# Kernel optimization log

Hardware: AMD Instinct MI355X
Metric: run time of the kernel (lower is better)

## Reference

```python
import jax, jax.numpy as jnp
import numpy as np

NEG = -1e30  # log-space 'zero' (avoid real -inf for stable exp/grad)


def _ctc_loss_mean(logp, targets, target_lengths, blank):
    """CTC loss, PyTorch semantics (reduction='mean', zero_infinity=True).
    logp: (B, T, V) log-probabilities; targets: (B, L) padded labels;
    target_lengths: (B,) ints. All input lengths are T (uniform here).
    """
    B, T, V = logp.shape
    L = targets.shape[1]
    S = 2 * L + 1  # extended label length: blank-interleaved

    ext = jnp.full((B, S), blank, dtype=targets.dtype)
    ext = ext.at[:, 1::2].set(targets)  # blanks at even s, labels at odd s

    s = jnp.arange(S)
    valid = s[None, :] < (2 * target_lengths + 1)[:, None]  # (B, S)
    prev2 = jnp.pad(ext[:, :-2], ((0, 0), (2, 0)), constant_values=blank)
    # skip transition s-2 -> s allowed only at non-blank s with no label repeat
    allow_skip = (s[None, :] >= 2) & (ext != blank) & (ext != prev2)

    # per-(t, s) emission log-prob, masked outside valid extended labels
    emit = jnp.take_along_axis(
        logp, jnp.broadcast_to(ext[:, None, :], (B, T, S)), axis=2
    )  # (B, T, S)
    emit = jnp.where(valid[:, None, :], emit, NEG)

    alpha0 = jnp.full((B, S), NEG, dtype=logp.dtype)
    alpha0 = alpha0.at[:, 0].set(emit[:, 0, 0])
    alpha0 = alpha0.at[:, 1].set(emit[:, 0, 1])

    def step(alpha, e):
        a1 = alpha
        a2 = jnp.pad(alpha[:, :-1], ((0, 0), (1, 0)), constant_values=NEG)
        a3 = jnp.pad(alpha[:, :-2], ((0, 0), (2, 0)), constant_values=NEG)
        a3 = jnp.where(allow_skip, a3, NEG)
        m = jnp.maximum(jnp.maximum(a1, a2), a3)
        new = m + jnp.log(jnp.exp(a1 - m) + jnp.exp(a2 - m) + jnp.exp(a3 - m)) + e
        return new, None

    alpha, _ = jax.lax.scan(step, alpha0, jnp.swapaxes(emit, 0, 1)[1:])

    i1 = (2 * target_lengths).astype(jnp.int32)
    l1 = jnp.take_along_axis(alpha, i1[:, None], axis=1)[:, 0]
    l2 = jnp.take_along_axis(alpha, jnp.maximum(i1 - 1, 0)[:, None], axis=1)[:, 0]
    l2 = jnp.where(target_lengths > 0, l2, NEG)
    m = jnp.maximum(l1, l2)
    loss = -(m + jnp.log(jnp.exp(l1 - m) + jnp.exp(l2 - m)))  # (B,)
    loss = jnp.where(loss > 1e20, 0.0, loss)  # zero_infinity=True
    # reduction='mean': divide by target length, then batch mean
    return jnp.mean(loss / jnp.maximum(target_lengths, 1).astype(loss.dtype))


def setup_inputs() -> dict:
    key = jax.random.key(0)
    kl, kt, kn = jax.random.split(key, 3)
    B, T, V, L = 32, 1024, 1000, 256
    logits = jax.random.normal(kl, (B, T, V), dtype=jnp.float32)
    targets = jax.random.randint(kt, (B, L), 1, V).astype(jnp.int32)
    lengths = jax.random.randint(kn, (B,), L // 2 + 2, L + 1)
    target_padding_mask = jnp.arange(L)[None, :] < lengths[:, None]  # bool (B, L)
    return {"logits": logits, "targets": targets,
            "target_padding_mask": target_padding_mask}


def reference(logits, targets, target_padding_mask):
    blank = 0
    lg = logits[:, :-1, :]            # drop last frame
    tgt = targets[:, 1:]              # drop leading (SOS) token
    logp = jax.nn.log_softmax(lg, axis=-1)  # (B, T-1, V)
    tlen = target_padding_mask.sum(axis=1).astype(jnp.int32) - 1
    return _ctc_loss_mean(logp, tgt, tlen, blank)
```

## Files before the change

### kernel.cpp

```cpp
#include <hip/hip_runtime.h>

#define LOG2E 1.4426950408889634f
#define LN2   0.6931471805599453

static constexpr int B  = 32;
static constexpr int T  = 1024;
static constexpr int TT = 1023;
static constexpr int V  = 1000;
static constexpr int L  = 256;
static constexpr int S  = 511;
static constexpr int SP = 512;
static constexpr int TP = 1024;

using h8  = __attribute__((ext_vector_type(8))) _Float16;
using hf2 = __attribute__((ext_vector_type(2))) __fp16;
using f4  = __attribute__((ext_vector_type(4))) float;
using i4  = __attribute__((ext_vector_type(4))) int;

__device__ __forceinline__ float fexp2(float x) {
#if __has_builtin(__builtin_amdgcn_exp2f)
  return __builtin_amdgcn_exp2f(x);
#else
  return exp2f(x);
#endif
}
__device__ __forceinline__ float flog2(float x) {
#if __has_builtin(__builtin_amdgcn_logf)
  return __builtin_amdgcn_logf(x);
#else
  return log2f(x);
#endif
}

#if __has_builtin(__builtin_amdgcn_update_dpp)
__device__ __forceinline__ float shr1f(float x) {
  int r = __builtin_amdgcn_update_dpp(0, __float_as_int(x), 0x138, 0xf, 0xf, true);
  return __int_as_float(r);
}
__device__ __forceinline__ int shl1i(int x) {
  return __builtin_amdgcn_update_dpp(0, x, 0x130, 0xf, 0xf, true);
}
#define DPP_SWITCH(T, OLD, SRC, BC)                                            \
  T r;                                                                         \
  switch (ctrl) {                                                              \
    case 0x111: r = __builtin_amdgcn_update_dpp(OLD, SRC, 0x111, 0xf, 0xf, BC); break; \
    case 0x112: r = __builtin_amdgcn_update_dpp(OLD, SRC, 0x112, 0xf, 0xf, BC); break; \
    case 0x114: r = __builtin_amdgcn_update_dpp(OLD, SRC, 0x114, 0xf, 0xf, BC); break; \
    case 0x118: r = __builtin_amdgcn_update_dpp(OLD, SRC, 0x118, 0xf, 0xf, BC); break; \
    case 0x142: r = __builtin_amdgcn_update_dpp(OLD, SRC, 0x142, 0xf, 0xf, BC); break; \
    default:    r = __builtin_amdgcn_update_dpp(OLD, SRC, 0x143, 0xf, 0xf, BC); break; \
  }

__device__ __forceinline__ int dppmax_step(int m, const int ctrl) {
  DPP_SWITCH(int, 0, m, true);
  return max(m, r);
}
__device__ __forceinline__ int wavemax_to_sgpr(int m) {
  m = dppmax_step(m, 0x111);
  m = dppmax_step(m, 0x112);
  m = dppmax_step(m, 0x114);
  m = dppmax_step(m, 0x118);
  m = dppmax_step(m, 0x142);
  m = dppmax_step(m, 0x143);
  return __builtin_amdgcn_readlane(m, 63);
}
__device__ __forceinline__ float dppfmax_step(float x, const int ctrl) {
  int xi = __float_as_int(x);
  DPP_SWITCH(int, xi, xi, false);
  return fmaxf(x, __int_as_float(r));
}
__device__ __forceinline__ float wavefmax(float x) {
  x = dppfmax_step(x, 0x111);
  x = dppfmax_step(x, 0x112);
  x = dppfmax_step(x, 0x114);
  x = dppfmax_step(x, 0x118);
  x = dppfmax_step(x, 0x142);
  x = dppfmax_step(x, 0x143);
  return __int_as_float(__builtin_amdgcn_readlane(__float_as_int(x), 63));
}
__device__ __forceinline__ float dppfadd_step(float x, const int ctrl) {
  DPP_SWITCH(int, 0, __float_as_int(x), true);
  return x + __int_as_float(r);
}
__device__ __forceinline__ float wavefsum(float x) {
  x = dppfadd_step(x, 0x111);
  x = dppfadd_step(x, 0x112);
  x = dppfadd_step(x, 0x114);
  x = dppfadd_step(x, 0x118);
  x = dppfadd_step(x, 0x142);
  x = dppfadd_step(x, 0x143);
  return __int_as_float(__builtin_amdgcn_readlane(__float_as_int(x), 63));
}
#else
__device__ __forceinline__ float shr1f(float x) {
  float r = __shfl_up(x, 1, 64);
  return (threadIdx.x & 63) == 0 ? 0.0f : r;
}
__device__ __forceinline__ int shl1i(int x) {
  int r = __shfl_down(x, 1, 64);
  return (threadIdx.x & 63) == 63 ? 0 : r;
}
__device__ __forceinline__ int wavemax_to_sgpr(int m) {
  for (int o = 32; o >= 1; o >>= 1) m = max(m, __shfl_xor(m, o, 64));
  return m;
}
__device__ __forceinline__ float wavefmax(float x) {
  for (int o = 32; o >= 1; o >>= 1) x = fmaxf(x, __shfl_xor(x, o, 64));
  return x;
}
__device__ __forceinline__ float wavefsum(float x) {
  for (int o = 32; o >= 1; o >>= 1) x += __shfl_xor(x, o, 64);
  return x;
}
#endif

__device__ __forceinline__ int mask_tlen(const unsigned char* maskb, int b, int lane) {
  int ca = 0;
  for (int k = lane; k < L; k += 64) ca += (maskb[b * L + k] != 0) ? 1 : 0;
  for (int o = 32; o >= 1; o >>= 1) ca += __shfl_xor(ca, o, 64);
  int cnt = ca;
  if (ca < 130) {
    const int* mi = (const int*)maskb;
    int cb = 0;
    for (int k = lane; k < L; k += 64) cb += (mi[b * L + k] != 0) ? 1 : 0;
    for (int o = 32; o >= 1; o >>= 1) cb += __shfl_xor(cb, o, 64);
    cnt = cb;
  }
  return cnt - 1;
}

__global__ __launch_bounds__(256) void k_emit(const float* __restrict__ logits,
                                              const int* __restrict__ targets,
                                              _Float16* __restrict__ E,
                                              float* __restrict__ G) {
  __shared__ float yrow[4][1024];
  const int wid = threadIdx.x >> 6;
  const int lane = threadIdx.x & 63;
  float* yw = yrow[wid];
  const int r = blockIdx.x * 4 + wid;
  const int b = r / TT;
  const int t = r - b * TT;

  const f4* row = reinterpret_cast<const f4*>(logits + ((size_t)b * T + t) * V);
  f4 u0 = row[lane];
  f4 u1 = row[lane + 64];
  f4 u2 = row[lane + 128];
  const bool has3 = (lane < 58);
  f4 u3;
  if (has3) u3 = row[lane + 192];
  else { u3[0] = u3[1] = u3[2] = u3[3] = -3.0e38f; }

  reinterpret_cast<f4*>(yw)[lane]       = u0;
  reinterpret_cast<f4*>(yw)[lane + 64]  = u1;
  reinterpret_cast<f4*>(yw)[lane + 128] = u2;
  if (has3) reinterpret_cast<f4*>(yw)[lane + 192] = u3;

  float lm = fmaxf(fmaxf(fmaxf(u0[0], u0[1]), fmaxf(u0[2], u0[3])),
                   fmaxf(fmaxf(u1[0], u1[1]), fmaxf(u1[2], u1[3])));
  lm = fmaxf(lm, fmaxf(fmaxf(u2[0], u2[1]), fmaxf(u2[2], u2[3])));
  lm = fmaxf(lm, fmaxf(fmaxf(u3[0], u3[1]), fmaxf(u3[2], u3[3])));
  const float my = wavefmax(lm);
  const float c = -my * LOG2E;

  float ps = fexp2(fmaf(u0[0], LOG2E, c)) + fexp2(fmaf(u0[1], LOG2E, c))
           + fexp2(fmaf(u0[2], LOG2E, c)) + fexp2(fmaf(u0[3], LOG2E, c))
           + fexp2(fmaf(u1[0], LOG2E, c)) + fexp2(fmaf(u1[1], LOG2E, c))
           + fexp2(fmaf(u1[2], LOG2E, c)) + fexp2(fmaf(u1[3], LOG2E, c))
           + fexp2(fmaf(u2[0], LOG2E, c)) + fexp2(fmaf(u2[1], LOG2E, c))
           + fexp2(fmaf(u2[2], LOG2E, c)) + fexp2(fmaf(u2[3], LOG2E, c))
           + fexp2(fmaf(u3[0], LOG2E, c)) + fexp2(fmaf(u3[1], LOG2E, c))
           + fexp2(fmaf(u3[2], LOG2E, c)) + fexp2(fmaf(u3[3], LOG2E, c));
  const float g = -flog2(wavefsum(ps));

  const int base = b * L + (lane << 2);
  i4 tv = *reinterpret_cast<const i4*>(targets + base);
  const int l1 = tv[1], l2 = tv[2], l3 = tv[3];
  const int l4 = shl1i(tv[0]);
  const float eb = fexp2(fmaf(yw[0],  LOG2E, c));
  const float e1 = fexp2(fmaf(yw[l1], LOG2E, c));
  const float e2 = fexp2(fmaf(yw[l2], LOG2E, c));
  const float e3 = fexp2(fmaf(yw[l3], LOG2E, c));
  float e4       = fexp2(fmaf(yw[l4], LOG2E, c));
  if (lane == 63) e4 = 0.0f;

#if __has_builtin(__builtin_amdgcn_cvt_pkrtz)
  i4 oi;
  { hf2 p = __builtin_amdgcn_cvt_pkrtz(eb, e1); oi[0] = __builtin_bit_cast(int, p); }
  { hf2 p = __builtin_amdgcn_cvt_pkrtz(eb, e2); oi[1] = __builtin_bit_cast(int, p); }
  { hf2 p = __builtin_amdgcn_cvt_pkrtz(eb, e3); oi[2] = __builtin_bit_cast(int, p); }
  { hf2 p = __builtin_amdgcn_cvt_pkrtz(eb, e4); oi[3] = __builtin_bit_cast(int, p); }
  reinterpret_cast<i4*>(E + ((size_t)b * TP + t) * SP)[lane] = oi;
#else
  h8 o;
  o[0] = (_Float16)eb; o[1] = (_Float16)e1;
  o[2] = (_Float16)eb; o[3] = (_Float16)e2;
  o[4] = (_Float16)eb; o[5] = (_Float16)e3;
  o[6] = (_Float16)eb; o[7] = (_Float16)e4;
  reinterpret_cast<h8*>(E + ((size_t)b * TP + t) * SP)[lane] = o;
#endif
  if (lane == 0) G[r] = g;
}

__global__ __launch_bounds__(64, 1) void k_ctc(const _Float16* __restrict__ E,
                                               const int* __restrict__ targets,
                                               const unsigned char* __restrict__ maskb,
                                               const float* __restrict__ G,
                                               float* __restrict__ lossb) {
  const int b = blockIdx.x;
  const int lane = threadIdx.x;
  const int s0 = lane << 3;
  const int* tg = targets + b * L;

  const int tl = mask_tlen(maskb, b, lane);

  double gs = 0.0;
  for (int k = lane; k < TT; k += 64) gs += (double)G[b * TT + k];
  for (int o = 32; o >= 1; o >>= 1) gs += __shfl_xor(gs, o, 64);

  float f1 = 0.0f, f3, f5, f7 = 0.0f;
  {
    int s = s0 + 1;
    if (s >= 3) f1 = (tg[(s + 1) >> 1] != tg[(s - 1) >> 1]) ? 1.0f : 0.0f;
    s = s0 + 3;
    f3 = (tg[(s + 1) >> 1] != tg[(s - 1) >> 1]) ? 1.0f : 0.0f;
    s = s0 + 5;
    f5 = (tg[(s + 1) >> 1] != tg[(s - 1) >> 1]) ? 1.0f : 0.0f;
    s = s0 + 7;
    if (s < S) f7 = (tg[(s + 1) >> 1] != tg[(s - 1) >> 1]) ? 1.0f : 0.0f;
  }

  const int s2t = 2 * tl;
  const int vm0 = (s0 + 0 <= s2t) ? -1 : 0;
  const int vm1 = (s0 + 1 <= s2t) ? -1 : 0;
  const int vm2 = (s0 + 2 <= s2t) ? -1 : 0;
  const int vm3 = (s0 + 3 <= s2t) ? -1 : 0;
  const int vm4 = (s0 + 4 <= s2t) ? -1 : 0;
  const int vm5 = (s0 + 5 <= s2t) ? -1 : 0;
  const int vm6 = (s0 + 6 <= s2t) ? -1 : 0;
  const int vm7 = (s0 + 7 <= s2t) ? -1 : 0;

  const _Float16* E0 = E + (size_t)b * TP * SP;
  const _Float16* Ebase = E0 + s0;

  float a0 = (lane == 0) ? (float)E0[0] : 0.0f;
  float a1 = (lane == 0) ? (float)E0[1] : 0.0f;
  float a2 = 0.f, a3 = 0.f, a4 = 0.f, a5 = 0.f, a6 = 0.f, a7 = 0.f;
  float n7 = 0.0f;
  int lsacc = 0;

  asm volatile("" :: "v"(f1), "v"(f3), "v"(f5), "v"(f7),
                     "v"(a0), "v"(a1), "v"(gs), "v"((float)tl));

#define GLROW4(d0, d1, d2, d3, p)                                \
  asm volatile("global_load_dwordx4 %0, %4, off\n\t"             \
               "global_load_dwordx4 %1, %4, off offset:1024\n\t" \
               "global_load_dwordx4 %2, %4, off offset:2048\n\t" \
               "global_load_dwordx4 %3, %4, off offset:3072"     \
               : "=&v"(d0), "=&v"(d1), "=&v"(d2), "=&v"(d3) : "v"(p))

#define LOAD8(P, r0)                                             \
  do {                                                           \
    const _Float16* q_ = Ebase + (size_t)(r0) * SP;              \
    GLROW4(P##0, P##1, P##2, P##3, q_);                          \
    GLROW4(P##4, P##5, P##6, P##7, q_ + 4 * SP);                 \
  } while (0)

#define VMWAIT8(n, P)                                            \
  do {                                                           \
    asm volatile("s_waitcnt vmcnt(" #n ")"                       \
                 : "+v"(P##0), "+v"(P##1), "+v"(P##2), "+v"(P##3), \
                   "+v"(P##4), "+v"(P##5), "+v"(P##6), "+v"(P##7)); \
    __builtin_amdgcn_sched_barrier(0);                           \
  } while (0)

#define MIXLO(D, SSS, HWORD)                                     \
  asm("v_fma_mix_f32 %0, %1, %2, 0 op_sel:[0,0,0] op_sel_hi:[0,1,0]" \
      : "=v"(D) : "v"(SSS), "v"(HWORD))
#define MIXHI(D, SSS, HWORD)                                     \
  asm("v_fma_mix_f32 %0, %1, %2, 0 op_sel:[0,1,0] op_sel_hi:[0,1,0]" \
      : "=v"(D) : "v"(SSS), "v"(HWORD))

#define STEPF(H)                                                \
  do {                                                          \
    i4 hw = __builtin_bit_cast(i4, (H));                        \
    float s7 = fmaf(f7, a5, a6 + a7);                           \
    float t7; MIXHI(t7, s7, hw[3]);                             \
    float n7n = shr1f(t7);                                      \
    float s0_ = a0 + n7;                                        \
    float s1_ = fmaf(f1, n7, a0 + a1);                          \
    float s2_ = a1 + a2;                                        \
    float s3_ = fmaf(f3, a1, a2 + a3);                          \
    float s4_ = a3 + a4;                                        \
    float s5_ = fmaf(f5, a3, a4 + a5);                          \
    float s6_ = a5 + a6;                                        \
    float t0, t1, t2, t3, t4, t5, t6;                           \
    MIXLO(t0, s0_, hw[0]);                                      \
    MIXHI(t1, s1_, hw[0]);                                      \
    MIXLO(t2, s2_, hw[1]);                                      \
    MIXHI(t3, s3_, hw[1]);                                      \
    MIXLO(t4, s4_, hw[2]);                                      \
    MIXHI(t5, s5_, hw[2]);                                      \
    MIXLO(t6, s6_, hw[3]);                                      \
    a0 = t0; a1 = t1; a2 = t2; a3 = t3;                         \
    a4 = t4; a5 = t5; a6 = t6; a7 = t7;                         \
    n7 = n7n;                                                   \
  } while (0)

#define RESCALE()                                               \
  do {                                                          \
    int m = max(max(max(__float_as_int(a0) & vm0,               \
                        __float_as_int(a1) & vm1),              \
                    max(__float_as_int(a2) & vm2,               \
                        __float_as_int(a3) & vm3)),             \
                max(max(__float_as_int(a4) & vm4,               \
                        __float_as_int(a5) & vm5),              \
                    max(__float_as_int(a6) & vm6,               \
                        __float_as_int(a7) & vm7)));            \
    int mw = wavemax_to_sgpr(m);                                \
    int e = mw >> 23;                                           \
    int sh = 191 - e;                                           \
    lsacc += e - 191;                                           \
    a0 = ldexpf(a0, sh); a1 = ldexpf(a1, sh);                   \
    a2 = ldexpf(a2, sh); a3 = ldexpf(a3, sh);                   \
    a4 = ldexpf(a4, sh); a5 = ldexpf(a5, sh);                   \
    a6 = ldexpf(a6, sh); a7 = ldexpf(a7, sh);                   \
    n7 = ldexpf(n7, sh);                                        \
  } while (0)

#define PROC8(P)                                                \
  do {                                                          \
    STEPF(P##0); STEPF(P##1); STEPF(P##2); STEPF(P##3);         \
    STEPF(P##4); STEPF(P##5); STEPF(P##6); STEPF(P##7);         \
  } while (0)

  h8 A0, A1, A2, A3, A4, A5, A6, A7;
  h8 B0, B1, B2, B3, B4, B5, B6, B7;
  h8 C0, C1, C2, C3, C4, C5, C6, C7;
  h8 D0, D1, D2, D3, D4, D5, D6, D7;

  LOAD8(A, 1);
  LOAD8(B, 9);
  LOAD8(C, 17);
  LOAD8(D, 25);

  int t = 1;
#pragma unroll 1
  for (int it = 0; it < 30; ++it) {
    RESCALE();
    VMWAIT8(24, A); PROC8(A); LOAD8(A, t + 32);
    VMWAIT8(24, B); PROC8(B); LOAD8(B, t + 40);
    VMWAIT8(24, C); PROC8(C); LOAD8(C, t + 48);
    VMWAIT8(24, D); PROC8(D); LOAD8(D, t + 56);
    t += 32;
  }
  RESCALE();
  VMWAIT8(24, A); PROC8(A); LOAD8(A, 993);
  VMWAIT8(24, B); PROC8(B); LOAD8(B, 1001);
  VMWAIT8(24, C); PROC8(C); LOAD8(C, 1009);
  VMWAIT8(24, D); PROC8(D); LOAD8(D, 1017);
  RESCALE();
  VMWAIT8(24, A); PROC8(A);
  VMWAIT8(16, B); PROC8(B);
  VMWAIT8(8,  C); PROC8(C);
  VMWAIT8(0,  D);
  STEPF(D0); STEPF(D1); STEPF(D2);
  STEPF(D3); STEPF(D4); STEPF(D5);
#undef GLROW4
#undef LOAD8
#undef VMWAIT8
#undef MIXLO
#undef MIXHI
#undef STEPF
#undef RESCALE
#undef PROC8

  {
    int i1 = 2 * tl;
    int j1 = (i1 > 0 ? i1 : 1) - 1;
    float va, vb;
    switch (i1 & 7) {
      case 0: va = a0; break; case 1: va = a1; break;
      case 2: va = a2; break; case 3: va = a3; break;
      case 4: va = a4; break; case 5: va = a5; break;
      case 6: va = a6; break; default: va = a7; break;
    }
    switch (j1 & 7) {
      case 0: vb = a0; break; case 1: vb = a1; break;
      case 2: vb = a2; break; case 3: vb = a3; break;
      case 4: vb = a4; break; case 5: vb = a5; break;
      case 6: vb = a6; break; default: vb = a7; break;
    }
    float l1v = __shfl(va, i1 >> 3, 64);
    float l2v = __shfl(vb, j1 >> 3, 64);
    if (lane == 0) {
      float p = l1v + l2v;
      int hi = __float_as_int(p);
      int ep = (hi >> 23) - 127;
      float pm = ldexpf(p, -ep);
      float lm = flog2(pm);
      double loss2 = -((double)lm + (double)ep + (double)lsacc + gs);
      float loss = (float)(loss2 * LN2);
      if (!(loss <= 1e20f)) loss = 0.0f;
      int dv = (tl > 0) ? tl : 1;
      lossb[b] = loss / (float)dv;
    }
  }
}

__global__ void k_mean(const float* __restrict__ lossb, float* __restrict__ out) {
  int lane = threadIdx.x;
  float v = (lane < B) ? lossb[lane] : 0.0f;
  for (int o = 32; o >= 1; o >>= 1) v += __shfl_xor(v, o, 64);
  if (lane == 0) out[0] = v / (float)B;
}

extern "C" void kernel_launch(void* const* d_in, const int* in_sizes, int n_in,
                              void* d_out, int out_size, void* d_ws, size_t ws_size,
                              hipStream_t stream) {
  const float* logits = (const float*)d_in[0];
  const int* targets = (const int*)d_in[1];
  const unsigned char* mask = (const unsigned char*)d_in[2];

  char* ws = (char*)d_ws;
  float* lossb = (float*)(ws + 128);
  float* G = (float*)(ws + 512);
  _Float16* E = (_Float16*)(ws + 512 + 132 * 1024);

  k_emit<<<(B * TT) / 4, 256, 0, stream>>>(logits, targets, E, G);
  k_ctc<<<B, 64, 0, stream>>>(E, targets, mask, G, lossb);
  k_mean<<<1, 64, 0, stream>>>(lossb, (float*)d_out);
}
```

Baseline: 84.41 us.

## Store blank emissions separately to halve emission buffer traffic

The emission buffer no longer interleaves a duplicated blank value with each label emission. It now keeps 256 label halves per row plus a compact per-time blank array and a small float array holding the t=0 initial values. The CTC recurrence loads dwordx2 label chunks together with one dwordx4 of blanks per 8 steps, and the wait counts and the step macros are updated to match. This cuts the bytes written by the emit kernel and read by the serial recurrence kernel, at the cost of more load instructions per block of steps. The G sum reduction is also moved after the recurrence loop so it is off the startup path.

```diff
diff --git a/kernel.cpp b/kernel.cpp
--- a/kernel.cpp
+++ b/kernel.cpp
@@ -9,13 +9,13 @@
 static constexpr int V  = 1000;
 static constexpr int L  = 256;
 static constexpr int S  = 511;
-static constexpr int SP = 512;
+static constexpr int LP = 256;
 static constexpr int TP = 1024;
 
-using h8  = __attribute__((ext_vector_type(8))) _Float16;
 using hf2 = __attribute__((ext_vector_type(2))) __fp16;
 using f4  = __attribute__((ext_vector_type(4))) float;
 using i4  = __attribute__((ext_vector_type(4))) int;
+using i2  = __attribute__((ext_vector_type(2))) int;
 
 __device__ __forceinline__ float fexp2(float x) {
 #if __has_builtin(__builtin_amdgcn_exp2f)
@@ -131,7 +131,9 @@
 
 __global__ __launch_bounds__(256) void k_emit(const float* __restrict__ logits,
                                               const int* __restrict__ targets,
-                                              _Float16* __restrict__ E,
+                                              _Float16* __restrict__ EL,
+                                              _Float16* __restrict__ EBs,
+                                              float* __restrict__ I2,
                                               float* __restrict__ G) {
   __shared__ float yrow[4][1024];
   const int wid = threadIdx.x >> 6;
@@ -183,28 +185,28 @@
   float e4       = fexp2(fmaf(yw[l4], LOG2E, c));
   if (lane == 63) e4 = 0.0f;
 
+  i2 oi;
 #if __has_builtin(__builtin_amdgcn_cvt_pkrtz)
-  i4 oi;
-  { hf2 p = __builtin_amdgcn_cvt_pkrtz(eb, e1); oi[0] = __builtin_bit_cast(int, p); }
-  { hf2 p = __builtin_amdgcn_cvt_pkrtz(eb, e2); oi[1] = __builtin_bit_cast(int, p); }
-  { hf2 p = __builtin_amdgcn_cvt_pkrtz(eb, e3); oi[2] = __builtin_bit_cast(int, p); }
-  { hf2 p = __builtin_amdgcn_cvt_pkrtz(eb, e4); oi[3] = __builtin_bit_cast(int, p); }
-  reinterpret_cast<i4*>(E + ((size_t)b * TP + t) * SP)[lane] = oi;
+  { hf2 p = __builtin_amdgcn_cvt_pkrtz(e1, e2); oi[0] = __builtin_bit_cast(int, p); }
+  { hf2 p = __builtin_amdgcn_cvt_pkrtz(e3, e4); oi[1] = __builtin_bit_cast(int, p); }
 #else
-  h8 o;
-  o[0] = (_Float16)eb; o[1] = (_Float16)e1;
-  o[2] = (_Float16)eb; o[3] = (_Float16)e2;
-  o[4] = (_Float16)eb; o[5] = (_Float16)e3;
-  o[6] = (_Float16)eb; o[7] = (_Float16)e4;
-  reinterpret_cast<h8*>(E + ((size_t)b * TP + t) * SP)[lane] = o;
+  { hf2 p; p[0] = (__fp16)e1; p[1] = (__fp16)e2; oi[0] = __builtin_bit_cast(int, p); }
+  { hf2 p; p[0] = (__fp16)e3; p[1] = (__fp16)e4; oi[1] = __builtin_bit_cast(int, p); }
 #endif
-  if (lane == 0) G[r] = g;
-}
-
-__global__ __launch_bounds__(64, 1) void k_ctc(const _Float16* __restrict__ E,
+  reinterpret_cast<i2*>(EL + ((size_t)b * TP + t) * LP)[lane] = oi;
+  if (lane == 0) {
+    G[r] = g;
+    if (t > 0) EBs[b * TP + (t - 1)] = (_Float16)eb;
+    else { I2[2 * b] = eb; I2[2 * b + 1] = e1; }
+  }
+}
+
+__global__ __launch_bounds__(64, 1) void k_ctc(const _Float16* __restrict__ EL,
+                                               const _Float16* __restrict__ EBs,
                                                const int* __restrict__ targets,
                                                const unsigned char* __restrict__ maskb,
                                                const float* __restrict__ G,
+                                               const float* __restrict__ I2,
                                                float* __restrict__ lossb) {
   const int b = blockIdx.x;
   const int lane = threadIdx.x;
@@ -212,10 +214,6 @@
   const int* tg = targets + b * L;
 
   const int tl = mask_tlen(maskb, b, lane);
-
-  double gs = 0.0;
-  for (int k = lane; k < TT; k += 64) gs += (double)G[b * TT + k];
-  for (int o = 32; o >= 1; o >>= 1) gs += __shfl_xor(gs, o, 64);
 
   float f1 = 0.0f, f3, f5, f7 = 0.0f;
   {
@@ -239,37 +237,44 @@
   const int vm6 = (s0 + 6 <= s2t) ? -1 : 0;
   const int vm7 = (s0 + 7 <= s2t) ? -1 : 0;
 
-  const _Float16* E0 = E + (size_t)b * TP * SP;
-  const _Float16* Ebase = E0 + s0;
-
-  float a0 = (lane == 0) ? (float)E0[0] : 0.0f;
-  float a1 = (lane == 0) ? (float)E0[1] : 0.0f;
+  const _Float16* ELb = EL + (size_t)b * TP * LP + (lane << 2);
+  const _Float16* EBb = EBs + b * TP;
+
+  float a0 = (lane == 0) ? I2[2 * b]     : 0.0f;
+  float a1 = (lane == 0) ? I2[2 * b + 1] : 0.0f;
   float a2 = 0.f, a3 = 0.f, a4 = 0.f, a5 = 0.f, a6 = 0.f, a7 = 0.f;
   float n7 = 0.0f;
   int lsacc = 0;
 
   asm volatile("" :: "v"(f1), "v"(f3), "v"(f5), "v"(f7),
-                     "v"(a0), "v"(a1), "v"(gs), "v"((float)tl));
-
-#define GLROW4(d0, d1, d2, d3, p)                                \
-  asm volatile("global_load_dwordx4 %0, %4, off\n\t"             \
-               "global_load_dwordx4 %1, %4, off offset:1024\n\t" \
-               "global_load_dwordx4 %2, %4, off offset:2048\n\t" \
-               "global_load_dwordx4 %3, %4, off offset:3072"     \
-               : "=&v"(d0), "=&v"(d1), "=&v"(d2), "=&v"(d3) : "v"(p))
+                     "v"(a0), "v"(a1), "v"((float)tl));
 
 #define LOAD8(P, r0)                                             \
   do {                                                           \
-    const _Float16* q_ = Ebase + (size_t)(r0) * SP;              \
-    GLROW4(P##0, P##1, P##2, P##3, q_);                          \
-    GLROW4(P##4, P##5, P##6, P##7, q_ + 4 * SP);                 \
+    const _Float16* ql_ = ELb + (size_t)(r0) * LP;               \
+    const _Float16* qb_ = EBb + ((r0) - 1);                      \
+    asm volatile(                                                \
+      "global_load_dwordx2 %0, %9, off\n\t"                      \
+      "global_load_dwordx2 %1, %9, off offset:512\n\t"           \
+      "global_load_dwordx2 %2, %9, off offset:1024\n\t"          \
+      "global_load_dwordx2 %3, %9, off offset:1536\n\t"          \
+      "global_load_dwordx2 %4, %9, off offset:2048\n\t"          \
+      "global_load_dwordx2 %5, %9, off offset:2560\n\t"          \
+      "global_load_dwordx2 %6, %9, off offset:3072\n\t"          \
+      "global_load_dwordx2 %7, %9, off offset:3584\n\t"          \
+      "global_load_dwordx4 %8, %10, off"                         \
+      : "=&v"(P##0), "=&v"(P##1), "=&v"(P##2), "=&v"(P##3),      \
+        "=&v"(P##4), "=&v"(P##5), "=&v"(P##6), "=&v"(P##7),      \
+        "=&v"(P##Q)                                              \
+      : "v"(ql_), "v"(qb_));                                     \
   } while (0)
 
 #define VMWAIT8(n, P)                                            \
   do {                                                           \
     asm volatile("s_waitcnt vmcnt(" #n ")"                       \
                  : "+v"(P##0), "+v"(P##1), "+v"(P##2), "+v"(P##3), \
-                   "+v"(P##4), "+v"(P##5), "+v"(P##6), "+v"(P##7)); \
+                   "+v"(P##4), "+v"(P##5), "+v"(P##6), "+v"(P##7), \
+                   "+v"(P##Q));                                  \
     __builtin_amdgcn_sched_barrier(0);                           \
   } while (0)
 
@@ -280,11 +285,10 @@
   asm("v_fma_mix_f32 %0, %1, %2, 0 op_sel:[0,1,0] op_sel_hi:[0,1,0]" \
       : "=v"(D) : "v"(SSS), "v"(HWORD))
 
-#define STEPF(H)                                                \
+#define STEP_IMPL(H, BD, BMIX)                                  \
   do {                                                          \
-    i4 hw = __builtin_bit_cast(i4, (H));                        \
-    float s7 = fmaf(f7, a5, a6 + a7);                           \
-    float t7; MIXHI(t7, s7, hw[3]);                             \
+    float s7_ = fmaf(f7, a5, a6 + a7);                          \
+    float t7; MIXHI(t7, s7_, (H)[1]);                   \
     float n7n = shr1f(t7);                                      \
     float s0_ = a0 + n7;                                        \
     float s1_ = fmaf(f1, n7, a0 + a1);                          \
@@ -294,17 +298,19 @@
     float s5_ = fmaf(f5, a3, a4 + a5);                          \
     float s6_ = a5 + a6;                                        \
     float t0, t1, t2, t3, t4, t5, t6;                           \
-    MIXLO(t0, s0_, hw[0]);                                      \
-    MIXHI(t1, s1_, hw[0]);                                      \
-    MIXLO(t2, s2_, hw[1]);                                      \
-    MIXHI(t3, s3_, hw[1]);                                      \
-    MIXLO(t4, s4_, hw[2]);                                      \
-    MIXHI(t5, s5_, hw[2]);                                      \
-    MIXLO(t6, s6_, hw[3]);                                      \
+    BMIX(t0, s0_, (BD));                             \
+    MIXLO(t1, s1_, (H)[0]);                             \
+    BMIX(t2, s2_, (BD));                                        \
+    MIXHI(t3, s3_, (H)[0]);                             \
+    BMIX(t4, s4_, (BD));                                        \
+    MIXLO(t5, s5_, (H)[1]);                             \
+    BMIX(t6, s6_, (BD));                                        \
     a0 = t0; a1 = t1; a2 = t2; a3 = t3;                         \
     a4 = t4; a5 = t5; a6 = t6; a7 = t7;                         \
     n7 = n7n;                                                   \
   } while (0)
+#define STEPFL(H, BD) STEP_IMPL(H, BD, MIXLO)
+#define STEPFH(H, BD) STEP_IMPL(H, BD, MIXHI)
 
 #define RESCALE()                                               \
   do {                                                          \
@@ -329,14 +335,16 @@
 
 #define PROC8(P)                                                \
   do {                                                          \
-    STEPF(P##0); STEPF(P##1); STEPF(P##2); STEPF(P##3);         \
-    STEPF(P##4); STEPF(P##5); STEPF(P##6); STEPF(P##7);         \
+    STEPFL(P##0, P##Q[0]); STEPFH(P##1, P##Q[0]);               \
+    STEPFL(P##2, P##Q[1]); STEPFH(P##3, P##Q[1]);               \
+    STEPFL(P##4, P##Q[2]); STEPFH(P##5, P##Q[2]);               \
+    STEPFL(P##6, P##Q[3]); STEPFH(P##7, P##Q[3]);               \
   } while (0)
 
-  h8 A0, A1, A2, A3, A4, A5, A6, A7;
-  h8 B0, B1, B2, B3, B4, B5, B6, B7;
-  h8 C0, C1, C2, C3, C4, C5, C6, C7;
-  h8 D0, D1, D2, D3, D4, D5, D6, D7;
+  i2 A0, A1, A2, A3, A4, A5, A6, A7; i4 AQ;
+  i2 B0, B1, B2, B3, B4, B5, B6, B7; i4 BQ;
+  i2 C0, C1, C2, C3, C4, C5, C6, C7; i4 CQ;
+  i2 D0, D1, D2, D3, D4, D5, D6, D7; i4 DQ;
 
   LOAD8(A, 1);
   LOAD8(B, 9);
@@ -347,32 +355,38 @@
 #pragma unroll 1
   for (int it = 0; it < 30; ++it) {
     RESCALE();
-    VMWAIT8(24, A); PROC8(A); LOAD8(A, t + 32);
-    VMWAIT8(24, B); PROC8(B); LOAD8(B, t + 40);
-    VMWAIT8(24, C); PROC8(C); LOAD8(C, t + 48);
-    VMWAIT8(24, D); PROC8(D); LOAD8(D, t + 56);
+    VMWAIT8(27, A); PROC8(A); LOAD8(A, t + 32);
+    VMWAIT8(27, B); PROC8(B); LOAD8(B, t + 40);
+    VMWAIT8(27, C); PROC8(C); LOAD8(C, t + 48);
+    VMWAIT8(27, D); PROC8(D); LOAD8(D, t + 56);
     t += 32;
   }
   RESCALE();
-  VMWAIT8(24, A); PROC8(A); LOAD8(A, 993);
-  VMWAIT8(24, B); PROC8(B); LOAD8(B, 1001);
-  VMWAIT8(24, C); PROC8(C); LOAD8(C, 1009);
-  VMWAIT8(24, D); PROC8(D); LOAD8(D, 1017);
+  VMWAIT8(27, A); PROC8(A); LOAD8(A, 993);
+  VMWAIT8(27, B); PROC8(B); LOAD8(B, 1001);
+  VMWAIT8(27, C); PROC8(C); LOAD8(C, 1009);
+  VMWAIT8(27, D); PROC8(D); LOAD8(D, 1017);
   RESCALE();
-  VMWAIT8(24, A); PROC8(A);
-  VMWAIT8(16, B); PROC8(B);
-  VMWAIT8(8,  C); PROC8(C);
+  VMWAIT8(27, A); PROC8(A);
+  VMWAIT8(18, B); PROC8(B);
+  VMWAIT8(9,  C); PROC8(C);
   VMWAIT8(0,  D);
-  STEPF(D0); STEPF(D1); STEPF(D2);
-  STEPF(D3); STEPF(D4); STEPF(D5);
-#undef GLROW4
+  STEPFL(D0, DQ[0]); STEPFH(D1, DQ[0]);
+  STEPFL(D2, DQ[1]); STEPFH(D3, DQ[1]);
+  STEPFL(D4, DQ[2]); STEPFH(D5, DQ[2]);
 #undef LOAD8
 #undef VMWAIT8
 #undef MIXLO
 #undef MIXHI
-#undef STEPF
+#undef STEP_IMPL
+#undef STEPFL
+#undef STEPFH
 #undef RESCALE
 #undef PROC8
+
+  double gs = 0.0;
+  for (int k = lane; k < TT; k += 64) gs += (double)G[b * TT + k];
+  for (int o = 32; o >= 1; o >>= 1) gs += __shfl_xor(gs, o, 64);
 
   {
     int i1 = 2 * tl;
@@ -423,10 +437,12 @@
 
   char* ws = (char*)d_ws;
   float* lossb = (float*)(ws + 128);
+  float* I2 = (float*)(ws + 256);
   float* G = (float*)(ws + 512);
-  _Float16* E = (_Float16*)(ws + 512 + 132 * 1024);
-
-  k_emit<<<(B * TT) / 4, 256, 0, stream>>>(logits, targets, E, G);
-  k_ctc<<<B, 64, 0, stream>>>(E, targets, mask, G, lossb);
+  _Float16* EBs = (_Float16*)(ws + 140 * 1024);
+  _Float16* EL = (_Float16*)(ws + 256 * 1024);
+
+  k_emit<<<(B * TT) / 4, 256, 0, stream>>>(logits, targets, EL, EBs, I2, G);
+  k_ctc<<<B, 64, 0, stream>>>(EL, EBs, targets, mask, G, I2, lossb);
   k_mean<<<1, 64, 0, stream>>>(lossb, (float*)d_out);
 }
```

Result: faster. 82.14 us (median of 3 runs) (-2.7%).
